# Optimization experiments

Hardware: AMD Instinct MI355X
Metric: run time of the kernel (lower is better)

The kernel has to match this reference:

```python
import jax, jax.numpy as jnp
import numpy as np

DIM = 512
HEADS = 8
AGENT = 49
POOL = 7  # int(sqrt(49))
EPS = 1e-5  # BatchNorm eps


def _adaptive_avg_pool(x, out_hw):
    # torch AdaptiveAvgPool2d semantics: bin i covers [floor(i*H/out), ceil((i+1)*H/out))
    B, C, H, W = x.shape
    cs = jnp.cumsum(jnp.cumsum(x, axis=2), axis=3)
    cs = jnp.pad(cs, ((0, 0), (0, 0), (1, 0), (1, 0)))  # integral image, [B,C,H+1,W+1]
    hs = np.floor(np.arange(out_hw) * H / out_hw).astype(np.int32)
    he = np.ceil((np.arange(out_hw) + 1) * H / out_hw).astype(np.int32)
    ws = np.floor(np.arange(out_hw) * W / out_hw).astype(np.int32)
    we = np.ceil((np.arange(out_hw) + 1) * W / out_hw).astype(np.int32)
    area = ((he - hs)[:, None] * (we - ws)[None, :]).astype(np.float32)
    s = (cs[:, :, he][:, :, :, we] - cs[:, :, hs][:, :, :, we]
         - cs[:, :, he][:, :, :, ws] + cs[:, :, hs][:, :, :, ws])
    return s / area


def setup_inputs() -> dict:
    key = jax.random.key(0)
    ks = jax.random.split(key, 8)
    d = DIM

    def w(k, shape, s=0.02):
        return jax.random.normal(k, shape, jnp.float32) * s

    return {
        "x": jax.random.normal(ks[0], (16, d, 32, 32), jnp.float32),
        "H": 32,
        "W": 32,
        "q_w": w(ks[1], (d, d)),
        "kv_w": w(ks[2], (2 * d, d)),
        "dw_w": w(ks[3], (d, 1, 3, 3), 0.1),   # depthwise 3x3, groups=d
        "dw_b": jnp.zeros((d,), jnp.float32),
        "bn_gamma": jnp.ones((d,), jnp.float32),
        "bn_beta": jnp.zeros((d,), jnp.float32),
        "bn_mean": jnp.zeros((d,), jnp.float32),
        "bn_var": jnp.ones((d,), jnp.float32),
        "pw_w": w(ks[4], (d, d, 1, 1)),          # pointwise 1x1 conv
        "pw_b": jnp.zeros((d,), jnp.float32),
        "proj_w": w(ks[5], (d, d)),
        "proj_b": jnp.zeros((d,), jnp.float32),
        "enh1_w": w(ks[6], (d, d)),
        "enh1_b": jnp.zeros((d,), jnp.float32),
        "enh2_w": w(ks[7], (d, d)),
        "enh2_b": jnp.zeros((d,), jnp.float32),
    }


def reference(x, H, W, q_w, kv_w, dw_w, dw_b, bn_gamma, bn_beta, bn_mean, bn_var,
              pw_w, pw_b, proj_w, proj_b, enh1_w, enh1_b, enh2_w, enh2_b):
    B, C, H, W = x.shape  # torch re-reads sizes from x
    N = H * W
    hd = C // HEADS
    scale = hd ** -0.5
    dn = ('NCHW', 'OIHW', 'NCHW')

    x_flat = x.reshape(B, C, N).transpose(0, 2, 1)            # [B,N,C]
    q = (x_flat @ q_w.T).reshape(B, N, HEADS, hd).transpose(0, 2, 1, 3)  # [B,h,N,hd]
    kv = (x_flat @ kv_w.T).reshape(B, N, 2, HEADS, hd).transpose(2, 0, 3, 1, 4)
    k, v = kv[0], kv[1]                                        # [B,h,N,hd]

    # agent tokens (faithful raw reshapes as in the torch code)
    a = _adaptive_avg_pool(x, POOL)                            # [B,C,7,7]
    a = a.reshape(B, C, AGENT).transpose(0, 2, 1)              # [B,49,C]
    a = a.reshape(B, C, POOL, POOL)                            # raw reshape (torch bug, kept)
    a = jax.lax.conv_general_dilated(a, dw_w, (1, 1), 'SAME',
                                     feature_group_count=C, dimension_numbers=dn)
    a = a + dw_b[None, :, None, None]
    a = (a - bn_mean[None, :, None, None]) * jax.lax.rsqrt(bn_var + EPS)[None, :, None, None]
    a = a * bn_gamma[None, :, None, None] + bn_beta[None, :, None, None]
    a = jax.nn.relu(a)
    a = jax.lax.conv_general_dilated(a, pw_w, (1, 1), 'SAME', dimension_numbers=dn)
    a = a + pw_b[None, :, None, None]
    a = a.reshape(B, AGENT, C)                                 # raw reshape
    a = a.reshape(B, HEADS, AGENT, hd)                         # raw reshape (torch bug, kept)

    # stage 1: agent <- kv
    agent_attn = jax.nn.softmax(jnp.einsum('bhad,bhnd->bhan', a, k) * scale, axis=-1)
    agg = jnp.einsum('bhan,bhnd->bhad', agent_attn, v)         # [B,h,49,hd]
    # stage 2: q <- agent
    q_attn = jax.nn.softmax(jnp.einsum('bhnd,bhad->bhna', q, a) * scale, axis=-1)
    enh = jnp.einsum('bhna,bhad->bhnd', q_attn, agg)           # [B,h,N,hd]
    enh = enh.transpose(0, 2, 1, 3).reshape(B, N, C)

    x_out = enh @ proj_w.T + proj_b
    out = (jax.nn.relu(x_out @ enh1_w.T + enh1_b) @ enh2_w.T + enh2_b) + x_out
    return out.reshape(B, C, H, W)  # raw reshape as in torch
```

## Files before the change

kernel.cpp:

```cpp
#include <hip/hip_runtime.h>
#include <stdint.h>


typedef float f32x4 __attribute__((ext_vector_type(4)));
typedef short s16x8 __attribute__((ext_vector_type(8)));

typedef __attribute__((address_space(1))) void glob_v;
typedef __attribute__((address_space(3))) void lds_v;
#define GLD16(g, l) \
  __builtin_amdgcn_global_load_lds((glob_v*)(g), (lds_v*)(l), 16, 0, 0)

__device__ __forceinline__ float bf2f(unsigned short u) {
  union { unsigned int i; float f; } v; v.i = ((unsigned int)u) << 16; return v.f;
}
__device__ __forceinline__ unsigned short f2bf(float f) {
  union { float f; unsigned int i; } v; v.f = f;
  return (unsigned short)((v.i + 0x7FFFu + ((v.i >> 16) & 1u)) >> 16);
}

__global__ __launch_bounds__(256) void k_transpose(const float* __restrict__ x,
                                                   unsigned short* __restrict__ xT) {
  __shared__ float tile[64][65];
  const int b = blockIdx.z, c0 = blockIdx.y * 64, n0 = blockIdx.x * 64;
  const int t = threadIdx.x, tn = t & 63, tg = t >> 6;
#pragma unroll
  for (int i = 0; i < 16; ++i) {
    const int c_l = tg * 16 + i;
    tile[c_l][tn] = x[(b * 512 + c0 + c_l) * 1024 + n0 + tn];
  }
  __syncthreads();
#pragma unroll
  for (int i = 0; i < 16; ++i) {
    const int n_l = tg * 16 + i;
    xT[(b * 1024 + n0 + n_l) * 512 + c0 + tn] = f2bf(tile[tn][n_l]);
  }
}

__global__ __launch_bounds__(256) void k_weights(
    const float* __restrict__ qw, const float* __restrict__ kvw,
    const float* __restrict__ pjw, const float* __restrict__ w1,
    const float* __restrict__ w2, unsigned short* __restrict__ Wqkv,
    unsigned short* __restrict__ Wpj, unsigned short* __restrict__ W1,
    unsigned short* __restrict__ W2) {
  const int u = blockIdx.x * 256 + threadIdx.x;
  const float* s; unsigned short* d; int su, du;
  if (u < 196608) { d = Wqkv; du = u;
    if (u < 65536) { s = qw; su = u; } else { s = kvw; su = u - 65536; } }
  else if (u < 262144) { s = pjw; su = u - 196608; d = Wpj; du = su; }
  else if (u < 327680) { s = w1; su = u - 262144; d = W1; du = su; }
  else { s = w2; su = u - 327680; d = W2; du = su; }
  const f32x4 val = ((const f32x4*)s)[su];
  uint2 pk;
  pk.x = (unsigned)f2bf(val[0]) | ((unsigned)f2bf(val[1]) << 16);
  pk.y = (unsigned)f2bf(val[2]) | ((unsigned)f2bf(val[3]) << 16);
  ((uint2*)d)[du] = pk;
}

__global__ __launch_bounds__(64) void k_pool(const float* __restrict__ x,
                                             float* __restrict__ p) {
  __shared__ float img[1024];
  const int bc = blockIdx.x, t = threadIdx.x;
  const float* src = x + bc * 1024;
#pragma unroll
  for (int i = 0; i < 16; ++i) img[t + 64 * i] = src[t + 64 * i];
  __syncthreads();
  if (t < 49) {
    const int i = t / 7, j = t % 7;
    const int hs = (i * 32) / 7, he = ((i + 1) * 32 + 6) / 7;
    const int ws = (j * 32) / 7, we = ((j + 1) * 32 + 6) / 7;
    float s = 0.f;
    for (int ii = hs; ii < he; ++ii)
      for (int jj = ws; jj < we; ++jj) s += img[ii * 32 + jj];
    p[bc * 49 + t] = s / (float)((he - hs) * (we - ws));
  }
}

__global__ __launch_bounds__(64) void k_dw(
    const float* __restrict__ p, const float* __restrict__ dww,
    const float* __restrict__ dwb, const float* __restrict__ g,
    const float* __restrict__ be, const float* __restrict__ mean,
    const float* __restrict__ var, float* __restrict__ r) {
  const int bc = blockIdx.x, t = threadIdx.x;
  if (t >= 49) return;
  const int b = bc >> 9, c = bc & 511;
  const int i = t / 7, j = t % 7;
  float sum = 0.f;
#pragma unroll
  for (int ki = 0; ki < 3; ++ki)
#pragma unroll
    for (int kj = 0; kj < 3; ++kj) {
      const int ii = i + ki - 1, jj = j + kj - 1;
      if (ii < 0 || ii > 6 || jj < 0 || jj > 6) continue;
      const int f = c * 49 + ii * 7 + jj;
      sum += dww[c * 9 + ki * 3 + kj] * p[(b * 512 + (f & 511)) * 49 + (f >> 9)];
    }
  sum += dwb[c];
  sum = (sum - mean[c]) * rsqrtf(var[c] + 1e-5f) * g[c] + be[c];
  r[bc * 49 + t] = fmaxf(sum, 0.f);
}

__global__ __launch_bounds__(256) void k_pw(const float* __restrict__ r,
                                            const float* __restrict__ w,
                                            const float* __restrict__ bias,
                                            float* __restrict__ A) {
  __shared__ float wl[128 * 36];
  __shared__ float rl[128 * 64];
  const int blk = blockIdx.x;
  const int b = blk >> 4, cg = blk & 15;
  const int t = threadIdx.x, wv = t >> 6, lane = t & 63;
  float acc[8];
#pragma unroll
  for (int j = 0; j < 8; ++j) acc[j] = 0.f;
  for (int ch = 0; ch < 4; ++ch) {
    __syncthreads();
#pragma unroll
    for (int u = t; u < 4096; u += 256) {
      const int co = u >> 7, ci = u & 127;
      wl[ci * 36 + co] = w[(cg * 32 + co) * 512 + ch * 128 + ci];
    }
    for (int u = t; u < 6272; u += 256) {
      const int ci = u / 49, s = u % 49;
      rl[ci * 64 + s] = r[b * 25088 + ch * 6272 + u];
    }
    __syncthreads();
#pragma unroll 4
    for (int ci = 0; ci < 128; ++ci) {
      const f32x4 w0 = *(const f32x4*)(wl + ci * 36 + wv * 8);
      const f32x4 w1 = *(const f32x4*)(wl + ci * 36 + wv * 8 + 4);
      const float rv = rl[ci * 64 + lane];
#pragma unroll
      for (int j = 0; j < 4; ++j) { acc[j] += w0[j] * rv; acc[4 + j] += w1[j] * rv; }
    }
  }
  if (lane < 49) {
#pragma unroll
    for (int j = 0; j < 8; ++j) {
      const int co = cg * 32 + wv * 8 + j;
      A[b * 25088 + co * 49 + lane] = acc[j] + bias[co];
    }
  }
}

template <int MODE>
__global__ __launch_bounds__(256) void k_gemm(
    const unsigned short* __restrict__ A, const unsigned short* __restrict__ B,
    unsigned short* __restrict__ oq, unsigned short* __restrict__ ok,
    unsigned short* __restrict__ ov, float* __restrict__ of,
    unsigned short* __restrict__ obf, const float* __restrict__ bias,
    const float* __restrict__ resid, float* __restrict__ dout) {
  __shared__ unsigned short As[2][4096];
  __shared__ unsigned short Bs[2][4096];
  const int t = threadIdx.x;
  constexpr int NB = (MODE == 0) ? 12 : 4;
  constexpr int NWG = NB * 128;
  const int swz = ((int)blockIdx.x & 7) * (NWG >> 3) + ((int)blockIdx.x >> 3);
  const int n0 = (swz % NB) * 128, m0 = (swz / NB) * 128;
  const int w = t >> 6, lane = t & 63;
  const int wr = w >> 1, wc = w & 1, lr = lane & 15, lg = lane >> 4;
  const int row = t >> 2, q = t & 3;
  const unsigned short* gA = A + m0 * 512;
  const unsigned short* gB = B + n0 * 512;

  auto stage = [&](int cur, int kt) {
    const unsigned short* sa = gA + row * 512 + kt * 32 + q * 8;
    const unsigned short* sb = gB + row * 512 + kt * 32 + q * 8;
    unsigned short* da = As[cur] + w * 512;
    unsigned short* db = Bs[cur] + w * 512;
    GLD16(sa, da);
    GLD16(sa + 32768, da + 2048);
    GLD16(sb, db);
    GLD16(sb + 32768, db + 2048);
  };

  f32x4 acc[4][4];
#pragma unroll
  for (int mi = 0; mi < 4; ++mi)
#pragma unroll
    for (int ni = 0; ni < 4; ++ni)
#pragma unroll
      for (int rr = 0; rr < 4; ++rr) acc[mi][ni][rr] = 0.f;

  stage(0, 0);
  __syncthreads();
  int cur = 0;
  for (int kt = 0; kt < 16; ++kt) {
    if (kt < 15) stage(cur ^ 1, kt + 1);
    const unsigned short* Ac = As[cur];
    const unsigned short* Bc = Bs[cur];
    s16x8 af[4], bfr[4];
#pragma unroll
    for (int mi = 0; mi < 4; ++mi)
      af[mi] = *(const s16x8*)(Ac + (wr * 64 + mi * 16 + lr) * 32 + lg * 8);
#pragma unroll
    for (int ni = 0; ni < 4; ++ni)
      bfr[ni] = *(const s16x8*)(Bc + (wc * 64 + ni * 16 + lr) * 32 + lg * 8);
#pragma unroll
    for (int mi = 0; mi < 4; ++mi)
#pragma unroll
      for (int ni = 0; ni < 4; ++ni)
        acc[mi][ni] = __builtin_amdgcn_mfma_f32_16x16x32_bf16(af[mi], bfr[ni],
                                                              acc[mi][ni], 0, 0, 0);
    __syncthreads();
    cur ^= 1;
  }

#pragma unroll
  for (int mi = 0; mi < 4; ++mi)
#pragma unroll
    for (int ni = 0; ni < 4; ++ni)
#pragma unroll
      for (int rr = 0; rr < 4; ++rr) {
        const int gm = m0 + wr * 64 + mi * 16 + lg * 4 + rr;
        const int gn = n0 + wc * 64 + ni * 16 + lr;
        const float val = acc[mi][ni][rr];
        if (MODE == 0) {
          const int b = gm >> 10, n = gm & 1023;
          const int hh = (gn >> 6) & 7, dd = gn & 63;
          const int idx = ((b * 8 + hh) * 1024 + n) * 64 + dd;
          const unsigned short bv = f2bf(val);
          if (gn < 512) oq[idx] = bv;
          else if (gn < 1024) ok[idx] = bv;
          else ov[idx] = bv;
        } else if (MODE == 1) {
          const float v2 = val + bias[gn];
          of[gm * 512 + gn] = v2;
          obf[gm * 512 + gn] = f2bf(v2);
        } else if (MODE == 2) {
          const float v2 = fmaxf(val + bias[gn], 0.f);
          obf[gm * 512 + gn] = f2bf(v2);
        } else {
          dout[gm * 512 + gn] = val + bias[gn] + resid[gm * 512 + gn];
        }
      }
}

__global__ __launch_bounds__(256) void k_aflash(
    const float* __restrict__ Abuf, const unsigned short* __restrict__ kbf,
    const unsigned short* __restrict__ vbf, float* __restrict__ numT,
    float* __restrict__ denG) {
  __shared__ unsigned short A_lds[64 * 72];
  __shared__ unsigned short K_lds[64 * 72];
  __shared__ unsigned short VT_lds[64 * 72];
  __shared__ unsigned short P_lds[64 * 72];
  const int blk = blockIdx.x;
  const int bh = blk >> 1, half = blk & 1;
  const int b = bh >> 3, h = bh & 7;
  const int t = threadIdx.x, w = t >> 6, lane = t & 63;
  const int lr = lane & 15, lg = lane >> 4;

  for (int u = t; u < 64 * 72; u += 256) A_lds[u] = 0;
  __syncthreads();
  for (int u = t; u < 3136; u += 256) {
    const int d = u / 49, ag = u % 49;
    A_lds[ag * 72 + d] = f2bf(Abuf[b * 25088 + (h * 64 + d) * 49 + ag]);
  }

  const unsigned short* kbase = kbf + bh * 65536 + half * 512 * 64;
  const unsigned short* vbase = vbf + bh * 65536 + half * 512 * 64;

  f32x4 num[4];
#pragma unroll
  for (int ni = 0; ni < 4; ++ni)
#pragma unroll
    for (int rr = 0; rr < 4; ++rr) num[ni][rr] = 0.f;
  float den[4] = {0.f, 0.f, 0.f, 0.f};

  for (int c = 0; c < 8; ++c) {
    const int n0 = c * 64;
    __syncthreads();
#pragma unroll
    for (int u = t; u < 512; u += 256) {
      const int rw = u >> 3, qq = u & 7;
      *(s16x8*)(K_lds + rw * 72 + qq * 8) =
          *(const s16x8*)(kbase + (n0 + rw) * 64 + qq * 8);
    }
#pragma unroll
    for (int u = t; u < 512; u += 256) {
      const int n_l = u & 63, qq = u >> 6;
      const s16x8 v = *(const s16x8*)(vbase + (n0 + n_l) * 64 + qq * 8);
#pragma unroll
      for (int j = 0; j < 8; ++j)
        VT_lds[(qq * 8 + j) * 72 + n_l] = (unsigned short)v[j];
    }
    __syncthreads();
    f32x4 s[4];
#pragma unroll
    for (int ni = 0; ni < 4; ++ni)
#pragma unroll
      for (int rr = 0; rr < 4; ++rr) s[ni][rr] = 0.f;
#pragma unroll
    for (int kk = 0; kk < 2; ++kk) {
      const s16x8 afr = *(const s16x8*)(A_lds + (w * 16 + lr) * 72 + kk * 32 + lg * 8);
#pragma unroll
      for (int ni = 0; ni < 4; ++ni) {
        const s16x8 bfr =
            *(const s16x8*)(K_lds + (ni * 16 + lr) * 72 + kk * 32 + lg * 8);
        s[ni] = __builtin_amdgcn_mfma_f32_16x16x32_bf16(afr, bfr, s[ni], 0, 0, 0);
      }
    }
#pragma unroll
    for (int ni = 0; ni < 4; ++ni)
#pragma unroll
      for (int rr = 0; rr < 4; ++rr) {
        const float p = __expf(s[ni][rr] * 0.125f);
        den[rr] += p;
        P_lds[(w * 16 + lg * 4 + rr) * 72 + ni * 16 + lr] = f2bf(p);
      }
#pragma unroll
    for (int kk = 0; kk < 2; ++kk) {
      const s16x8 pa = *(const s16x8*)(P_lds + (w * 16 + lr) * 72 + kk * 32 + lg * 8);
#pragma unroll
      for (int ni = 0; ni < 4; ++ni) {
        const s16x8 vfr =
            *(const s16x8*)(VT_lds + (ni * 16 + lr) * 72 + kk * 32 + lg * 8);
        num[ni] = __builtin_amdgcn_mfma_f32_16x16x32_bf16(pa, vfr, num[ni], 0, 0, 0);
      }
    }
  }
#pragma unroll
  for (int rr = 0; rr < 4; ++rr) {
#pragma unroll
    for (int o = 1; o < 16; o <<= 1) den[rr] += __shfl_xor(den[rr], o, 64);
  }
  const int obase = (half * 128 + bh) * 4096;
#pragma unroll
  for (int ni = 0; ni < 4; ++ni)
    *(f32x4*)(numT + obase + (ni * 16 + lr) * 64 + w * 16 + lg * 4) = num[ni];
  if (lr == 0) {
    f32x4 dv;
#pragma unroll
    for (int rr = 0; rr < 4; ++rr) dv[rr] = den[rr];
    *(f32x4*)(denG + (half * 128 + bh) * 64 + w * 16 + lg * 4) = dv;
  }
}

__global__ __launch_bounds__(256) void k_attn2(
    const float* __restrict__ Abuf, const float* __restrict__ numT,
    const float* __restrict__ denG, const unsigned short* __restrict__ qbf,
    unsigned short* __restrict__ enh) {
  __shared__ unsigned short A_lds[64 * 72];
  __shared__ unsigned short G_lds[64 * 72];
  __shared__ unsigned short P2_lds[4][64 * 72];
  __shared__ float den_lds[64];
  const int blk = blockIdx.x;
  const int bh = blk >> 2, nq = blk & 3;
  const int b = bh >> 3, h = bh & 7;
  const int t = threadIdx.x, w = t >> 6, lane = t & 63;
  const int lr = lane & 15, lg = lane >> 4;

  if (t < 64) den_lds[t] = 1.f / (denG[bh * 64 + t] + denG[8192 + bh * 64 + t]);
  for (int u = t; u < 64 * 72; u += 256) A_lds[u] = 0;
  __syncthreads();
  for (int u = t; u < 3136; u += 256) {
    const int d = u / 49, ag = u % 49;
    A_lds[ag * 72 + d] = f2bf(Abuf[b * 25088 + (h * 64 + d) * 49 + ag]);
  }
  for (int u = t; u < 4096; u += 256) {
    const int d = u >> 6, ag = u & 63;
    const float v = (numT[bh * 4096 + u] + numT[524288 + bh * 4096 + u]) * den_lds[ag];
    G_lds[d * 72 + ag] = f2bf(v);
  }
  __syncthreads();

  const int nbase = nq * 256 + w * 64;
  const unsigned short* qp = qbf + (bh * 1024 + nbase) * 64;
  s16x8 qf[4][2];
#pragma unroll
  for (int mi = 0; mi < 4; ++mi)
#pragma unroll
    for (int kk = 0; kk < 2; ++kk)
      qf[mi][kk] = *(const s16x8*)(qp + (mi * 16 + lr) * 64 + kk * 32 + lg * 8);

  f32x4 L[4][4];
#pragma unroll
  for (int mi = 0; mi < 4; ++mi)
#pragma unroll
    for (int ni = 0; ni < 4; ++ni)
#pragma unroll
      for (int rr = 0; rr < 4; ++rr) L[mi][ni][rr] = 0.f;
#pragma unroll
  for (int kk = 0; kk < 2; ++kk)
#pragma unroll
    for (int ni = 0; ni < 4; ++ni) {
      const s16x8 bfr = *(const s16x8*)(A_lds + (ni * 16 + lr) * 72 + kk * 32 + lg * 8);
#pragma unroll
      for (int mi = 0; mi < 4; ++mi)
        L[mi][ni] = __builtin_amdgcn_mfma_f32_16x16x32_bf16(qf[mi][kk], bfr,
                                                            L[mi][ni], 0, 0, 0);
    }
  unsigned short* pw = P2_lds[w];
#pragma unroll
  for (int mi = 0; mi < 4; ++mi) {
    float ps[4][4];
    float rs[4];
#pragma unroll
    for (int rr = 0; rr < 4; ++rr) rs[rr] = 0.f;
#pragma unroll
    for (int ni = 0; ni < 4; ++ni) {
      const bool valid = (ni < 3) | (lr == 0);
#pragma unroll
      for (int rr = 0; rr < 4; ++rr) {
        const float p = valid ? __expf(L[mi][ni][rr] * 0.125f) : 0.f;
        ps[ni][rr] = p;
        rs[rr] += p;
      }
    }
#pragma unroll
    for (int rr = 0; rr < 4; ++rr) {
#pragma unroll
      for (int o = 1; o < 16; o <<= 1) rs[rr] += __shfl_xor(rs[rr], o, 64);
      rs[rr] = 1.f / rs[rr];
    }
#pragma unroll
    for (int ni = 0; ni < 4; ++ni)
#pragma unroll
      for (int rr = 0; rr < 4; ++rr)
        pw[(mi * 16 + lg * 4 + rr) * 72 + ni * 16 + lr] = f2bf(ps[ni][rr] * rs[rr]);
  }
#pragma unroll
  for (int mi = 0; mi < 4; ++mi) {
    f32x4 e[4];
#pragma unroll
    for (int ni = 0; ni < 4; ++ni)
#pragma unroll
      for (int rr = 0; rr < 4; ++rr) e[ni][rr] = 0.f;
#pragma unroll
    for (int kk = 0; kk < 2; ++kk) {
      const s16x8 pa = *(const s16x8*)(pw + (mi * 16 + lr) * 72 + kk * 32 + lg * 8);
#pragma unroll
      for (int ni = 0; ni < 4; ++ni) {
        const s16x8 gb = *(const s16x8*)(G_lds + (ni * 16 + lr) * 72 + kk * 32 + lg * 8);
        e[ni] = __builtin_amdgcn_mfma_f32_16x16x32_bf16(pa, gb, e[ni], 0, 0, 0);
      }
    }
#pragma unroll
    for (int ni = 0; ni < 4; ++ni)
#pragma unroll
      for (int rr = 0; rr < 4; ++rr) {
        const int n = nbase + mi * 16 + lg * 4 + rr;
        enh[(b * 1024 + n) * 512 + h * 64 + ni * 16 + lr] = f2bf(e[ni][rr]);
      }
  }
}

extern "C" void kernel_launch(void* const* d_in, const int* in_sizes, int n_in,
                              void* d_out, int out_size, void* d_ws, size_t ws_size,
                              hipStream_t stream) {
  const float* x    = (const float*)d_in[0];
  const float* q_w  = (const float*)d_in[3];
  const float* kv_w = (const float*)d_in[4];
  const float* dw_w = (const float*)d_in[5];
  const float* dw_b = (const float*)d_in[6];
  const float* bn_g = (const float*)d_in[7];
  const float* bn_b = (const float*)d_in[8];
  const float* bn_m = (const float*)d_in[9];
  const float* bn_v = (const float*)d_in[10];
  const float* pw_w = (const float*)d_in[11];
  const float* pw_b = (const float*)d_in[12];
  const float* pj_w = (const float*)d_in[13];
  const float* pj_b = (const float*)d_in[14];
  const float* e1_w = (const float*)d_in[15];
  const float* e1_b = (const float*)d_in[16];
  const float* e2_w = (const float*)d_in[17];
  const float* e2_b = (const float*)d_in[18];

  char* base = (char*)d_ws;
  size_t off = 0;
  auto alloc = [&](size_t bytes) -> void* {
    void* r = base + off;
    off += (bytes + 255) & ~(size_t)255;
    return r;
  };
  unsigned short* Wqkv = (unsigned short*)alloc(786432ull * 2);
  unsigned short* Wpj  = (unsigned short*)alloc(262144ull * 2);
  unsigned short* W1   = (unsigned short*)alloc(262144ull * 2);
  unsigned short* W2   = (unsigned short*)alloc(262144ull * 2);
  unsigned short* xT   = (unsigned short*)alloc(8388608ull * 2);
  unsigned short* qb   = (unsigned short*)alloc(8388608ull * 2);
  unsigned short* kb   = (unsigned short*)alloc(8388608ull * 2);
  unsigned short* vb   = (unsigned short*)alloc(8388608ull * 2);
  float* pbuf = (float*)alloc(401408ull * 4);
  float* rbuf = (float*)alloc(401408ull * 4);
  float* Abuf = (float*)alloc(401408ull * 4);
  float* numT = (float*)alloc(1048576ull * 4);
  float* denG = (float*)alloc(16384ull * 4);
  unsigned short* enh  = (unsigned short*)alloc(8388608ull * 2);
  float* xout = (float*)alloc(8388608ull * 4);
  unsigned short* xoutb = (unsigned short*)alloc(8388608ull * 2);
  unsigned short* h1    = (unsigned short*)alloc(8388608ull * 2);
  (void)ws_size; (void)in_sizes; (void)n_in; (void)out_size;

  k_weights<<<1536, 256, 0, stream>>>(q_w, kv_w, pj_w, e1_w, e2_w, Wqkv, Wpj, W1, W2);
  k_transpose<<<dim3(16, 8, 16), 256, 0, stream>>>(x, xT);
  k_pool<<<8192, 64, 0, stream>>>(x, pbuf);
  k_dw<<<8192, 64, 0, stream>>>(pbuf, dw_w, dw_b, bn_g, bn_b, bn_m, bn_v, rbuf);
  k_pw<<<256, 256, 0, stream>>>(rbuf, pw_w, pw_b, Abuf);
  k_gemm<0><<<1536, 256, 0, stream>>>(xT, Wqkv, qb, kb, vb,
                                      nullptr, nullptr, nullptr, nullptr, nullptr);
  k_aflash<<<256, 256, 0, stream>>>(Abuf, kb, vb, numT, denG);
  k_attn2<<<512, 256, 0, stream>>>(Abuf, numT, denG, qb, enh);
  k_gemm<1><<<512, 256, 0, stream>>>(enh, Wpj, nullptr, nullptr, nullptr,
                                     xout, xoutb, pj_b, nullptr, nullptr);
  k_gemm<2><<<512, 256, 0, stream>>>(xoutb, W1, nullptr, nullptr, nullptr,
                                     nullptr, h1, e1_b, nullptr, nullptr);
  k_gemm<3><<<512, 256, 0, stream>>>(h1, W2, nullptr, nullptr, nullptr,
                                     nullptr, nullptr, e2_b, xout, (float*)d_out);
}
```

Baseline: 210.0 us.

## Restructure GEMM into 256x128 ping-pong pipeline and fuse pooling into transpose

The bf16 GEMM kernel moves from 128x128 tiles with 256 threads to 256x128 tiles with 512 threads. Its K step grows to 64 with XOR-swizzled LDS layout, and four sub-tile loads are interleaved with MFMA groups under explicit vmcnt waits, barriers and setprio, so global-to-LDS copies overlap compute. Separately, the adaptive avg pool no longer re-reads x in its own kernel. The transpose kernel emits per-row partial column-bin sums from its LDS tile, and a small reduction kernel finishes the pooling. The risks are a more fragile hand-tuned wait-count schedule, higher register and LDS pressure, and an extra intermediate buffer plus launch.

```diff
diff --git a/kernel.cpp b/kernel.cpp
--- a/kernel.cpp
+++ b/kernel.cpp
@@ -9,6 +9,8 @@
 typedef __attribute__((address_space(3))) void lds_v;
 #define GLD16(g, l) \
   __builtin_amdgcn_global_load_lds((glob_v*)(g), (lds_v*)(l), 16, 0, 0)
+#define VMCNT(N) asm volatile("s_waitcnt vmcnt(" #N ")" ::: "memory")
+#define BAR() __builtin_amdgcn_s_barrier()
 
 __device__ __forceinline__ float bf2f(unsigned short u) {
   union { unsigned int i; float f; } v; v.i = ((unsigned int)u) << 16; return v.f;
@@ -18,8 +20,12 @@
   return (unsigned short)((v.i + 0x7FFFu + ((v.i >> 16) & 1u)) >> 16);
 }
 
+__constant__ int ws7[7] = {0, 4, 9, 13, 18, 22, 27};
+__constant__ int we7[7] = {5, 10, 14, 19, 23, 28, 32};
+
 __global__ __launch_bounds__(256) void k_transpose(const float* __restrict__ x,
-                                                   unsigned short* __restrict__ xT) {
+                                                   unsigned short* __restrict__ xT,
+                                                   float* __restrict__ p_rows) {
   __shared__ float tile[64][65];
   const int b = blockIdx.z, c0 = blockIdx.y * 64, n0 = blockIdx.x * 64;
   const int t = threadIdx.x, tn = t & 63, tg = t >> 6;
@@ -34,6 +40,30 @@
     const int n_l = tg * 16 + i;
     xT[(b * 1024 + n0 + n_l) * 512 + c0 + tn] = f2bf(tile[tn][n_l]);
   }
+  if (t < 128) {
+    const int c_l = t >> 1, rw = t & 1;
+    const int rowg = blockIdx.x * 2 + rw;
+    const float* src = &tile[c_l][rw * 32];
+    float* dst = p_rows + ((b * 512 + c0 + c_l) * 32 + rowg) * 8;
+#pragma unroll
+    for (int jb = 0; jb < 7; ++jb) {
+      float s = 0.f;
+      for (int cc = ws7[jb]; cc < we7[jb]; ++cc) s += src[cc];
+      dst[jb] = s;
+    }
+  }
+}
+
+__global__ __launch_bounds__(256) void k_poolred(const float* __restrict__ p_rows,
+                                                 float* __restrict__ p) {
+  const int u = blockIdx.x * 256 + threadIdx.x;
+  if (u >= 401408) return;
+  const int bc = u / 49, ij = u % 49;
+  const int i = ij / 7, j = ij % 7;
+  float s = 0.f;
+  for (int r = ws7[i]; r < we7[i]; ++r) s += p_rows[bc * 256 + r * 8 + j];
+  const float area = (float)((we7[i] - ws7[i]) * (we7[j] - ws7[j]));
+  p[u] = s / area;
 }
 
 __global__ __launch_bounds__(256) void k_weights(
@@ -56,25 +86,6 @@
   ((uint2*)d)[du] = pk;
 }
 
-__global__ __launch_bounds__(64) void k_pool(const float* __restrict__ x,
-                                             float* __restrict__ p) {
-  __shared__ float img[1024];
-  const int bc = blockIdx.x, t = threadIdx.x;
-  const float* src = x + bc * 1024;
-#pragma unroll
-  for (int i = 0; i < 16; ++i) img[t + 64 * i] = src[t + 64 * i];
-  __syncthreads();
-  if (t < 49) {
-    const int i = t / 7, j = t % 7;
-    const int hs = (i * 32) / 7, he = ((i + 1) * 32 + 6) / 7;
-    const int ws = (j * 32) / 7, we = ((j + 1) * 32 + 6) / 7;
-    float s = 0.f;
-    for (int ii = hs; ii < he; ++ii)
-      for (int jj = ws; jj < we; ++jj) s += img[ii * 32 + jj];
-    p[bc * 49 + t] = s / (float)((he - hs) * (we - ws));
-  }
-}
-
 __global__ __launch_bounds__(64) void k_dw(
     const float* __restrict__ p, const float* __restrict__ dww,
     const float* __restrict__ dwb, const float* __restrict__ g,
@@ -142,96 +153,136 @@
 }
 
 template <int MODE>
-__global__ __launch_bounds__(256) void k_gemm(
+__global__ __launch_bounds__(512, 2) void k_gemm(
     const unsigned short* __restrict__ A, const unsigned short* __restrict__ B,
     unsigned short* __restrict__ oq, unsigned short* __restrict__ ok,
     unsigned short* __restrict__ ov, float* __restrict__ of,
     unsigned short* __restrict__ obf, const float* __restrict__ bias,
     const float* __restrict__ resid, float* __restrict__ dout) {
-  __shared__ unsigned short As[2][4096];
-  __shared__ unsigned short Bs[2][4096];
+  __shared__ unsigned short lA[2][2][128 * 64];
+  __shared__ unsigned short lB[2][2][64 * 64];
   const int t = threadIdx.x;
   constexpr int NB = (MODE == 0) ? 12 : 4;
-  constexpr int NWG = NB * 128;
+  constexpr int NWG = NB * 64;
   const int swz = ((int)blockIdx.x & 7) * (NWG >> 3) + ((int)blockIdx.x >> 3);
-  const int n0 = (swz % NB) * 128, m0 = (swz / NB) * 128;
-  const int w = t >> 6, lane = t & 63;
-  const int wr = w >> 1, wc = w & 1, lr = lane & 15, lg = lane >> 4;
-  const int row = t >> 2, q = t & 3;
+  const int n0 = (swz % NB) * 128, m0 = (swz / NB) * 256;
+  const int wid = t >> 6, lane = t & 63;
+  const int wm = wid >> 2, wn = wid & 3;
+  const int lr = lane & 15, lg = lane >> 4;
   const unsigned short* gA = A + m0 * 512;
   const unsigned short* gB = B + n0 * 512;
 
-  auto stage = [&](int cur, int kt) {
-    const unsigned short* sa = gA + row * 512 + kt * 32 + q * 8;
-    const unsigned short* sb = gB + row * 512 + kt * 32 + q * 8;
-    unsigned short* da = As[cur] + w * 512;
-    unsigned short* db = Bs[cur] + w * 512;
-    GLD16(sa, da);
-    GLD16(sa + 32768, da + 2048);
-    GLD16(sb, db);
-    GLD16(sb + 32768, db + 2048);
+  auto stageA = [&](int bi, int mh, int kt) {
+#pragma unroll
+    for (int c = 0; c < 2; ++c) {
+      const int G = c * 512 + t;
+      const int row = G >> 3, s = G & 7;
+      const unsigned short* src =
+          gA + (mh * 128 + row) * 512 + kt * 64 + ((s ^ (row & 7)) << 3);
+      GLD16(src, &lA[bi][mh][0] + G * 8);
+    }
   };
-
-  f32x4 acc[4][4];
-#pragma unroll
-  for (int mi = 0; mi < 4; ++mi)
-#pragma unroll
-    for (int ni = 0; ni < 4; ++ni)
-#pragma unroll
-      for (int rr = 0; rr < 4; ++rr) acc[mi][ni][rr] = 0.f;
-
-  stage(0, 0);
-  __syncthreads();
-  int cur = 0;
-  for (int kt = 0; kt < 16; ++kt) {
-    if (kt < 15) stage(cur ^ 1, kt + 1);
-    const unsigned short* Ac = As[cur];
-    const unsigned short* Bc = Bs[cur];
-    s16x8 af[4], bfr[4];
+  auto stageB = [&](int bi, int nh, int kt) {
+    const int col = t >> 3, s = t & 7;
+    const unsigned short* src =
+        gB + (nh * 64 + col) * 512 + kt * 64 + ((s ^ (col & 7)) << 3);
+    GLD16(src, &lB[bi][nh][0] + t * 8);
+  };
+  s16x8 af[8], bf[2];
+  auto readA = [&](int bi, int mh) {
 #pragma unroll
     for (int mi = 0; mi < 4; ++mi)
-      af[mi] = *(const s16x8*)(Ac + (wr * 64 + mi * 16 + lr) * 32 + lg * 8);
-#pragma unroll
-    for (int ni = 0; ni < 4; ++ni)
-      bfr[ni] = *(const s16x8*)(Bc + (wc * 64 + ni * 16 + lr) * 32 + lg * 8);
+#pragma unroll
+      for (int kk = 0; kk < 2; ++kk) {
+        const int row = wm * 64 + mi * 16 + lr;
+        const int g = (kk * 4 + lg) ^ (row & 7);
+        af[mi * 2 + kk] = *(const s16x8*)(&lA[bi][mh][0] + row * 64 + g * 8);
+      }
+  };
+  auto readB = [&](int bi, int nh) {
+#pragma unroll
+    for (int kk = 0; kk < 2; ++kk) {
+      const int col = wn * 16 + lr;
+      const int g = (kk * 4 + lg) ^ (col & 7);
+      bf[kk] = *(const s16x8*)(&lB[bi][nh][0] + col * 64 + g * 8);
+    }
+  };
+  f32x4 acc[2][2][4];
+#pragma unroll
+  for (int mh = 0; mh < 2; ++mh)
+#pragma unroll
+    for (int nh = 0; nh < 2; ++nh)
+#pragma unroll
+      for (int mi = 0; mi < 4; ++mi)
+#pragma unroll
+        for (int rr = 0; rr < 4; ++rr) acc[mh][nh][mi][rr] = 0.f;
+  auto mfma8 = [&](f32x4* ac) {
+    __builtin_amdgcn_s_setprio(1);
 #pragma unroll
     for (int mi = 0; mi < 4; ++mi)
 #pragma unroll
-      for (int ni = 0; ni < 4; ++ni)
-        acc[mi][ni] = __builtin_amdgcn_mfma_f32_16x16x32_bf16(af[mi], bfr[ni],
-                                                              acc[mi][ni], 0, 0, 0);
-    __syncthreads();
-    cur ^= 1;
-  }
-
-#pragma unroll
-  for (int mi = 0; mi < 4; ++mi)
-#pragma unroll
-    for (int ni = 0; ni < 4; ++ni)
-#pragma unroll
-      for (int rr = 0; rr < 4; ++rr) {
-        const int gm = m0 + wr * 64 + mi * 16 + lg * 4 + rr;
-        const int gn = n0 + wc * 64 + ni * 16 + lr;
-        const float val = acc[mi][ni][rr];
-        if (MODE == 0) {
-          const int b = gm >> 10, n = gm & 1023;
-          const int hh = (gn >> 6) & 7, dd = gn & 63;
-          const int idx = ((b * 8 + hh) * 1024 + n) * 64 + dd;
-          const unsigned short bv = f2bf(val);
-          if (gn < 512) oq[idx] = bv;
-          else if (gn < 1024) ok[idx] = bv;
-          else ov[idx] = bv;
-        } else if (MODE == 1) {
-          const float v2 = val + bias[gn];
-          of[gm * 512 + gn] = v2;
-          obf[gm * 512 + gn] = f2bf(v2);
-        } else if (MODE == 2) {
-          const float v2 = fmaxf(val + bias[gn], 0.f);
-          obf[gm * 512 + gn] = f2bf(v2);
-        } else {
-          dout[gm * 512 + gn] = val + bias[gn] + resid[gm * 512 + gn];
+      for (int kk = 0; kk < 2; ++kk)
+        ac[mi] = __builtin_amdgcn_mfma_f32_16x16x32_bf16(af[mi * 2 + kk], bf[kk],
+                                                         ac[mi], 0, 0, 0);
+    __builtin_amdgcn_s_setprio(0);
+  };
+
+  stageA(0, 0, 0); stageB(0, 0, 0); stageB(0, 1, 0); stageA(0, 1, 0);
+
+  for (int kt = 0; kt < 7; ++kt) {
+    const int bi = kt & 1, bn = bi ^ 1;
+    stageA(bn, 0, kt + 1);
+    VMCNT(5); BAR();
+    readA(bi, 0); readB(bi, 0);
+    mfma8(acc[0][0]); BAR();
+    stageB(bn, 0, kt + 1);
+    VMCNT(5); BAR();
+    readB(bi, 1);
+    mfma8(acc[0][1]); BAR();
+    stageB(bn, 1, kt + 1);
+    VMCNT(4); BAR();
+    readA(bi, 1); readB(bi, 0);
+    mfma8(acc[1][0]); BAR();
+    stageA(bn, 1, kt + 1);
+    BAR();
+    readB(bi, 1);
+    mfma8(acc[1][1]); BAR();
+  }
+  VMCNT(3); BAR(); readA(1, 0); readB(1, 0); mfma8(acc[0][0]); BAR();
+  VMCNT(2); BAR(); readB(1, 1); mfma8(acc[0][1]); BAR();
+  VMCNT(0); BAR(); readA(1, 1); readB(1, 0); mfma8(acc[1][0]); BAR();
+  readB(1, 1); mfma8(acc[1][1]);
+
+#pragma unroll
+  for (int mh = 0; mh < 2; ++mh)
+#pragma unroll
+    for (int nh = 0; nh < 2; ++nh)
+#pragma unroll
+      for (int mi = 0; mi < 4; ++mi)
+#pragma unroll
+        for (int rr = 0; rr < 4; ++rr) {
+          const int gm = m0 + mh * 128 + wm * 64 + mi * 16 + lg * 4 + rr;
+          const int gn = n0 + nh * 64 + wn * 16 + lr;
+          const float val = acc[mh][nh][mi][rr];
+          if (MODE == 0) {
+            const int b = gm >> 10, n = gm & 1023;
+            const int hh = (gn >> 6) & 7, dd = gn & 63;
+            const int idx = ((b * 8 + hh) * 1024 + n) * 64 + dd;
+            const unsigned short bv = f2bf(val);
+            if (gn < 512) oq[idx] = bv;
+            else if (gn < 1024) ok[idx] = bv;
+            else ov[idx] = bv;
+          } else if (MODE == 1) {
+            const float v2 = val + bias[gn];
+            of[gm * 512 + gn] = v2;
+            obf[gm * 512 + gn] = f2bf(v2);
+          } else if (MODE == 2) {
+            const float v2 = fmaxf(val + bias[gn], 0.f);
+            obf[gm * 512 + gn] = f2bf(v2);
+          } else {
+            dout[gm * 512 + gn] = val + bias[gn] + resid[gm * 512 + gn];
+          }
         }
-      }
 }
 
 __global__ __launch_bounds__(256) void k_aflash(
@@ -479,6 +530,7 @@
   unsigned short* qb   = (unsigned short*)alloc(8388608ull * 2);
   unsigned short* kb   = (unsigned short*)alloc(8388608ull * 2);
   unsigned short* vb   = (unsigned short*)alloc(8388608ull * 2);
+  float* prow = (float*)alloc(2097152ull * 4);
   float* pbuf = (float*)alloc(401408ull * 4);
   float* rbuf = (float*)alloc(401408ull * 4);
   float* Abuf = (float*)alloc(401408ull * 4);
@@ -491,18 +543,18 @@
   (void)ws_size; (void)in_sizes; (void)n_in; (void)out_size;
 
   k_weights<<<1536, 256, 0, stream>>>(q_w, kv_w, pj_w, e1_w, e2_w, Wqkv, Wpj, W1, W2);
-  k_transpose<<<dim3(16, 8, 16), 256, 0, stream>>>(x, xT);
-  k_pool<<<8192, 64, 0, stream>>>(x, pbuf);
+  k_transpose<<<dim3(16, 8, 16), 256, 0, stream>>>(x, xT, prow);
+  k_poolred<<<1568, 256, 0, stream>>>(prow, pbuf);
   k_dw<<<8192, 64, 0, stream>>>(pbuf, dw_w, dw_b, bn_g, bn_b, bn_m, bn_v, rbuf);
   k_pw<<<256, 256, 0, stream>>>(rbuf, pw_w, pw_b, Abuf);
-  k_gemm<0><<<1536, 256, 0, stream>>>(xT, Wqkv, qb, kb, vb,
-                                      nullptr, nullptr, nullptr, nullptr, nullptr);
+  k_gemm<0><<<768, 512, 0, stream>>>(xT, Wqkv, qb, kb, vb,
+                                     nullptr, nullptr, nullptr, nullptr, nullptr);
   k_aflash<<<256, 256, 0, stream>>>(Abuf, kb, vb, numT, denG);
   k_attn2<<<512, 256, 0, stream>>>(Abuf, numT, denG, qb, enh);
-  k_gemm<1><<<512, 256, 0, stream>>>(enh, Wpj, nullptr, nullptr, nullptr,
+  k_gemm<1><<<256, 512, 0, stream>>>(enh, Wpj, nullptr, nullptr, nullptr,
                                      xout, xoutb, pj_b, nullptr, nullptr);
-  k_gemm<2><<<512, 256, 0, stream>>>(xoutb, W1, nullptr, nullptr, nullptr,
+  k_gemm<2><<<256, 512, 0, stream>>>(xoutb, W1, nullptr, nullptr, nullptr,
                                      nullptr, h1, e1_b, nullptr, nullptr);
-  k_gemm<3><<<512, 256, 0, stream>>>(h1, W2, nullptr, nullptr, nullptr,
+  k_gemm<3><<<256, 512, 0, stream>>>(h1, W2, nullptr, nullptr, nullptr,
                                      nullptr, nullptr, e2_b, xout, (float*)d_out);
 }
```

Result: slower. 214.4 us (+2.1%).

## Fuse adaptive pooling row sums into transpose kernel and repack depthwise blocks

Applied to the files above, without the earlier changes.

The transpose kernel already holds each 64x64 tile of x in shared memory. It now also writes per-row partial sums over the seven pooling column bins to a new buffer. A small reduction kernel then combines rows into the 7x7 pooled output, so the separate pool kernel no longer re-reads all of x (32 MB). The depthwise kernel is also repacked from 64-thread blocks to 256-thread blocks holding four channels each. This adds one extra launch and an 8 MB intermediate buffer.

```diff
diff --git a/kernel.cpp b/kernel.cpp
--- a/kernel.cpp
+++ b/kernel.cpp
@@ -18,8 +18,12 @@
   return (unsigned short)((v.i + 0x7FFFu + ((v.i >> 16) & 1u)) >> 16);
 }
 
+__constant__ int ws7[7] = {0, 4, 9, 13, 18, 22, 27};
+__constant__ int we7[7] = {5, 10, 14, 19, 23, 28, 32};
+
 __global__ __launch_bounds__(256) void k_transpose(const float* __restrict__ x,
-                                                   unsigned short* __restrict__ xT) {
+                                                   unsigned short* __restrict__ xT,
+                                                   float* __restrict__ p_rows) {
   __shared__ float tile[64][65];
   const int b = blockIdx.z, c0 = blockIdx.y * 64, n0 = blockIdx.x * 64;
   const int t = threadIdx.x, tn = t & 63, tg = t >> 6;
@@ -34,6 +38,30 @@
     const int n_l = tg * 16 + i;
     xT[(b * 1024 + n0 + n_l) * 512 + c0 + tn] = f2bf(tile[tn][n_l]);
   }
+  if (t < 128) {
+    const int c_l = t >> 1, rw = t & 1;
+    const int rowg = blockIdx.x * 2 + rw;
+    const float* src = &tile[c_l][rw * 32];
+    float* dst = p_rows + ((b * 512 + c0 + c_l) * 32 + rowg) * 8;
+#pragma unroll
+    for (int jb = 0; jb < 7; ++jb) {
+      float s = 0.f;
+      for (int cc = ws7[jb]; cc < we7[jb]; ++cc) s += src[cc];
+      dst[jb] = s;
+    }
+  }
+}
+
+__global__ __launch_bounds__(256) void k_poolred(const float* __restrict__ p_rows,
+                                                 float* __restrict__ p) {
+  const int u = blockIdx.x * 256 + threadIdx.x;
+  if (u >= 401408) return;
+  const int bc = u / 49, ij = u % 49;
+  const int i = ij / 7, j = ij % 7;
+  float s = 0.f;
+  for (int r = ws7[i]; r < we7[i]; ++r) s += p_rows[bc * 256 + r * 8 + j];
+  const float area = (float)((we7[i] - ws7[i]) * (we7[j] - ws7[j]));
+  p[u] = s / area;
 }
 
 __global__ __launch_bounds__(256) void k_weights(
@@ -56,34 +84,16 @@
   ((uint2*)d)[du] = pk;
 }
 
-__global__ __launch_bounds__(64) void k_pool(const float* __restrict__ x,
-                                             float* __restrict__ p) {
-  __shared__ float img[1024];
-  const int bc = blockIdx.x, t = threadIdx.x;
-  const float* src = x + bc * 1024;
-#pragma unroll
-  for (int i = 0; i < 16; ++i) img[t + 64 * i] = src[t + 64 * i];
-  __syncthreads();
-  if (t < 49) {
-    const int i = t / 7, j = t % 7;
-    const int hs = (i * 32) / 7, he = ((i + 1) * 32 + 6) / 7;
-    const int ws = (j * 32) / 7, we = ((j + 1) * 32 + 6) / 7;
-    float s = 0.f;
-    for (int ii = hs; ii < he; ++ii)
-      for (int jj = ws; jj < we; ++jj) s += img[ii * 32 + jj];
-    p[bc * 49 + t] = s / (float)((he - hs) * (we - ws));
-  }
-}
-
-__global__ __launch_bounds__(64) void k_dw(
+__global__ __launch_bounds__(256) void k_dw(
     const float* __restrict__ p, const float* __restrict__ dww,
     const float* __restrict__ dwb, const float* __restrict__ g,
     const float* __restrict__ be, const float* __restrict__ mean,
     const float* __restrict__ var, float* __restrict__ r) {
-  const int bc = blockIdx.x, t = threadIdx.x;
-  if (t >= 49) return;
+  const int t = threadIdx.x, s = t & 63;
+  if (s >= 49) return;
+  const int bc = blockIdx.x * 4 + (t >> 6);
   const int b = bc >> 9, c = bc & 511;
-  const int i = t / 7, j = t % 7;
+  const int i = s / 7, j = s % 7;
   float sum = 0.f;
 #pragma unroll
   for (int ki = 0; ki < 3; ++ki)
@@ -96,7 +106,7 @@
     }
   sum += dwb[c];
   sum = (sum - mean[c]) * rsqrtf(var[c] + 1e-5f) * g[c] + be[c];
-  r[bc * 49 + t] = fmaxf(sum, 0.f);
+  r[bc * 49 + s] = fmaxf(sum, 0.f);
 }
 
 __global__ __launch_bounds__(256) void k_pw(const float* __restrict__ r,
@@ -479,6 +489,7 @@
   unsigned short* qb   = (unsigned short*)alloc(8388608ull * 2);
   unsigned short* kb   = (unsigned short*)alloc(8388608ull * 2);
   unsigned short* vb   = (unsigned short*)alloc(8388608ull * 2);
+  float* prow = (float*)alloc(2097152ull * 4);
   float* pbuf = (float*)alloc(401408ull * 4);
   float* rbuf = (float*)alloc(401408ull * 4);
   float* Abuf = (float*)alloc(401408ull * 4);
@@ -491,9 +502,9 @@
   (void)ws_size; (void)in_sizes; (void)n_in; (void)out_size;
 
   k_weights<<<1536, 256, 0, stream>>>(q_w, kv_w, pj_w, e1_w, e2_w, Wqkv, Wpj, W1, W2);
-  k_transpose<<<dim3(16, 8, 16), 256, 0, stream>>>(x, xT);
-  k_pool<<<8192, 64, 0, stream>>>(x, pbuf);
-  k_dw<<<8192, 64, 0, stream>>>(pbuf, dw_w, dw_b, bn_g, bn_b, bn_m, bn_v, rbuf);
+  k_transpose<<<dim3(16, 8, 16), 256, 0, stream>>>(x, xT, prow);
+  k_poolred<<<1568, 256, 0, stream>>>(prow, pbuf);
+  k_dw<<<2048, 256, 0, stream>>>(pbuf, dw_w, dw_b, bn_g, bn_b, bn_m, bn_v, rbuf);
   k_pw<<<256, 256, 0, stream>>>(rbuf, pw_w, pw_b, Abuf);
   k_gemm<0><<<1536, 256, 0, stream>>>(xT, Wqkv, qb, kb, vb,
                                       nullptr, nullptr, nullptr, nullptr, nullptr);
```

Result: no change. 211.0 us (+0.5%).
